# Kernel optimization log

Measured on AMD Instinct MI355X. Metric: run time of the kernel, lower is better.

Reference implementation:

```python
import jax, jax.numpy as jnp
import numpy as np
from itertools import permutations, combinations

BATCH = 32768
EPS = 1e-06  # positivity eps from __init__


def _levi_civita7():
    e = np.zeros((7,) * 7, dtype=np.float32)
    for p in permutations(range(7)):
        inv = sum(1 for i in range(7) for j in range(i + 1, 7) if p[i] > p[j])
        e[p] = -1.0 if inv % 2 else 1.0
    return jnp.asarray(e)

_EPS7 = _levi_civita7()  # (7,7,7,7,7,7,7) rank-7 Levi-Civita tensor
_TRIPLES = np.array(list(combinations(range(7), 3)), dtype=np.int32)  # (35,3) i<j<k index triples
_PERMS3 = [((0, 1, 2), 1.0), ((1, 2, 0), 1.0), ((2, 0, 1), 1.0),
           ((0, 2, 1), -1.0), ((2, 1, 0), -1.0), ((1, 0, 2), -1.0)]


def _phi_full(phi):
    # expand 35 independent components to fully antisymmetric (B,7,7,7)
    b = phi.shape[0]
    pf = jnp.zeros((b, 7, 7, 7), phi.dtype)
    for perm, s in _PERMS3:
        ia = _TRIPLES[:, perm[0]]
        ib = _TRIPLES[:, perm[1]]
        ic = _TRIPLES[:, perm[2]]
        pf = pf.at[:, ia, ib, ic].set(s * phi)
    return pf


def _metric_from_phi(phi):
    # Standard G2 metric: B_ij = (1/144) phi_ikl phi_jmn phi_pqr eps^{klmnpqr};
    # g = B / |det B|^{1/9}  (unit-determinant normalization)
    pf = _phi_full(phi)  # (B,7,7,7)
    C = jnp.einsum('klmnpqr,bpqr->bklmn', _EPS7, pf)  # (B,7,7,7,7)
    T = jnp.einsum('bklmn,bjmn->bklj', C, pf)          # (B,7,7,7)
    Bm = jnp.einsum('bikl,bklj->bij', pf, T) / 144.0   # (B,7,7)
    det = jnp.linalg.det(Bm)
    g = Bm / (jnp.abs(det)[:, None, None] + 1e-12) ** (1.0 / 9.0)
    return 0.5 * (g + jnp.swapaxes(g, -1, -2))  # exact symmetry for eigvalsh


def setup_inputs() -> dict:
    key = jax.random.key(0)
    phi = jax.random.normal(key, (BATCH, 35), dtype=jnp.float32)
    return {"phi": phi}


def reference(phi):
    g = _metric_from_phi(phi)              # (B,7,7)
    ev = jnp.linalg.eigvalsh(g)            # (B,7)
    return jax.nn.relu(-ev + EPS).sum(axis=-1)  # (B,) sum of negative-eigenvalue violations
```

## Files before the change

kernel.cpp:

```cpp
#include <hip/hip_runtime.h>
#include <utility>

#define BATCH 32768
#define NPHI 35
#define SWEEPS 6

constexpr int choose2(int n){ return (n*(n-1))/2; }

constexpr int tri_id_sorted(int a,int b,int c){
  int id=0;
  for(int x=0;x<a;++x) id += choose2(6-x);
  for(int y=a+1;y<b;++y) id += (6-y);
  id += (c-b-1);
  return id;
}

constexpr int tri_id3(int a,int b,int c){
  int x=a,y=b,z=c;
  if (x>y){int t=x;x=y;y=t;}
  if (y>z){int t=y;y=z;z=t;}
  if (x>y){int t=x;x=y;y=t;}
  return tri_id_sorted(x,y,z);
}

constexpr int sgn3(int a,int b,int c){
  int inv = (a>b)+(a>c)+(b>c);
  return (inv&1)? -1 : 1;
}

constexpr int UT(int i,int j){
  return i*7 - (i*(i-1))/2 + (j-i);
}

constexpr int pair_k(int g){
  int idx=0;
  for(int k=0;k<7;++k) for(int l=k+1;l<7;++l){ if(idx==g) return k; ++idx; }
  return 0;
}
constexpr int pair_l(int g){
  int idx=0;
  for(int k=0;k<7;++k) for(int l=k+1;l<7;++l){ if(idx==g) return l; ++idx; }
  return 0;
}

constexpr int rr_p(int r,int s){ int a=(r+1+s)%7, b=(r+6-s)%7; return a<b?a:b; }
constexpr int rr_q(int r,int s){ int a=(r+1+s)%7, b=(r+6-s)%7; return a<b?b:a; }

struct GProg {
  int nt, nb;
  signed char t_dst[50], t_a[50], t_b[50], t_s[50]; unsigned char t_init[50];
  signed char b_dst[26], b_a[26], b_b[26], b_s[26];
};

constexpr GProg build_group(int k,int l){
  GProg P{}; P.nt=0; P.nb=0;
  bool tinit[7]={};
  for(int m=0;m<7;++m) for(int n2=m+1;n2<7;++n2){
    if(m==k||m==l||n2==k||n2==l) continue;
    int comp[3]={0,0,0}; int cn=0;
    for(int x=0;x<7;++x) if(x!=k&&x!=l&&x!=m&&x!=n2){ comp[cn]=x; ++cn; }
    int perm[7]={k,l,m,n2,comp[0],comp[1],comp[2]};
    int invc=0;
    for(int i=0;i<7;++i) for(int j=i+1;j<7;++j) if(perm[i]>perm[j]) ++invc;
    const int es=(invc&1)? -1 : 1;
    const int tcomp=tri_id_sorted(comp[0],comp[1],comp[2]);
    for(int j=0;j<7;++j){
      if(j==m||j==n2) continue;
      P.t_dst[P.nt]=(signed char)j;
      P.t_a [P.nt]=(signed char)tcomp;
      P.t_b [P.nt]=(signed char)tri_id3(j,m,n2);
      P.t_s [P.nt]=(signed char)(es*sgn3(j,m,n2));
      P.t_init[P.nt]=tinit[j]?0:1; tinit[j]=true;
      ++P.nt;
    }
  }
  for(int i=0;i<7;++i){
    if(i==k||i==l) continue;
    for(int j=i;j<7;++j){
      P.b_dst[P.nb]=(signed char)UT(i,j);
      P.b_a [P.nb]=(signed char)tri_id3(i,k,l);
      P.b_b [P.nb]=(signed char)j;
      P.b_s [P.nb]=(signed char)sgn3(i,k,l);
      ++P.nb;
    }
  }
  return P;
}

template<int G> inline constexpr GProg GP = build_group(pair_k(G), pair_l(G));

template<int G,int Q>
__device__ __forceinline__ void t_step(float (&T)[7], const float (&ph)[NPHI]){
  constexpr int d=GP<G>.t_dst[Q], a=GP<G>.t_a[Q], b=GP<G>.t_b[Q];
  constexpr bool neg=(GP<G>.t_s[Q]<0), ini=(GP<G>.t_init[Q]!=0);
  const float x = neg ? -ph[a] : ph[a];
  if constexpr (ini) T[d] = x*ph[b];
  else               T[d] = fmaf(x, ph[b], T[d]);
}

template<int G,int Q>
__device__ __forceinline__ void b_step(float (&U)[28], const float (&T)[7],
                                       const float (&ph)[NPHI]){
  constexpr int d=GP<G>.b_dst[Q], a=GP<G>.b_a[Q], b=GP<G>.b_b[Q];
  constexpr bool neg=(GP<G>.b_s[Q]<0);
  const float x = neg ? -ph[a] : ph[a];
  U[d] = fmaf(x, T[b], U[d]);
}

template<int G,int... TQ>
__device__ __forceinline__ void run_t(float (&T)[7], const float (&ph)[NPHI],
                                      std::integer_sequence<int,TQ...>){
  (t_step<G,TQ>(T,ph), ...);
}
template<int G,int... BQ>
__device__ __forceinline__ void run_b(float (&U)[28], const float (&T)[7],
                                      const float (&ph)[NPHI],
                                      std::integer_sequence<int,BQ...>){
  (b_step<G,BQ>(U,T,ph), ...);
}

template<int G>
__device__ __forceinline__ void do_group(float (&U)[28], const float (&ph)[NPHI]){
  float T[7];
  run_t<G>(T, ph, std::make_integer_sequence<int, GP<G>.nt>{});
  run_b<G>(U, T, ph, std::make_integer_sequence<int, GP<G>.nb>{});
  __builtin_amdgcn_sched_barrier(0);
}

template<int... G>
__device__ __forceinline__ void all_groups(float (&U)[28], const float (&ph)[NPHI],
                                           std::integer_sequence<int,G...>){
  (do_group<G>(U,ph), ...);
}

template<int P,int Q>
__device__ __forceinline__ void jangle(const float (&A)[28],
                                       float &t, float &c, float &s){
  const float apq = A[UT(P,Q)];
  const float app = A[UT(P,P)];
  const float aqq = A[UT(Q,Q)];
  const float s2  = apq + apq;
  const float h   = aqq - app;
  const float r   = __builtin_amdgcn_sqrtf(fmaf(s2, s2, h*h));
  const float den = h + __builtin_copysignf(r + 1e-38f, h);
  t = s2 * __builtin_amdgcn_rcpf(den);
  c = __builtin_amdgcn_rsqf(fmaf(t, t, 1.0f));
  s = t*c;
}

template<int P,int Q>
__device__ __forceinline__ void japply(float (&A)[28], float t, float c, float s){
  const float apq = A[UT(P,Q)];
  A[UT(P,P)] = fmaf(-t, apq, A[UT(P,P)]);
  A[UT(Q,Q)] = fmaf( t, apq, A[UT(Q,Q)]);
  A[UT(P,Q)] = 0.0f;
  #pragma unroll
  for (int r2=0;r2<7;++r2){
    if (r2==P || r2==Q) continue;
    const int irp = (r2<P)? UT(r2,P) : UT(P,r2);
    const int irq = (r2<Q)? UT(r2,Q) : UT(Q,r2);
    const float arp = A[irp], arq = A[irq];
    A[irp] = fmaf(c, arp, -(s*arq));
    A[irq] = fmaf(c, arq,  (s*arp));
  }
}

template<int R>
__device__ __forceinline__ void jround(float (&A)[28]){
  constexpr int p0=rr_p(R,0), q0=rr_q(R,0);
  constexpr int p1=rr_p(R,1), q1=rr_q(R,1);
  constexpr int p2=rr_p(R,2), q2=rr_q(R,2);
  float t0,c0,s0, t1,c1,s1, t2,c2,s2;
  jangle<p0,q0>(A, t0,c0,s0);
  jangle<p1,q1>(A, t1,c1,s1);
  jangle<p2,q2>(A, t2,c2,s2);
  japply<p0,q0>(A, t0,c0,s0);
  japply<p1,q1>(A, t1,c1,s1);
  japply<p2,q2>(A, t2,c2,s2);
}

template<int... R>
__device__ __forceinline__ void jsweep(float (&A)[28],
                                       std::integer_sequence<int,R...>){
  (jround<R>(A), ...);
}

__device__ __forceinline__ float finish(const float (&A)[28]){
  float det = 1.0f;
  #pragma unroll
  for (int i=0;i<7;++i) det *= A[UT(i,i)];
  const float ad = fabsf(det) + 1e-12f;
  const float scale = __builtin_amdgcn_exp2f(__builtin_amdgcn_logf(ad) * (1.0f/9.0f));
  const float inv = __builtin_amdgcn_rcpf(scale);
  float sum = 0.0f;
  #pragma unroll
  for (int i=0;i<7;++i){
    const float ev = A[UT(i,i)]*inv;
    sum += fmaxf(1e-6f - ev, 0.0f);
  }
  return sum;
}

__global__ __launch_bounds__(64,1)
void PositivityConstraint_89086211654295_kernel(const float* __restrict__ phi,
                                                float* __restrict__ out){
  const int lane = threadIdx.x;
  const int gid  = blockIdx.x*64 + lane;

  __shared__ float lph[64*36];
  const float* __restrict__ gbase = phi + (size_t)blockIdx.x * 64 * NPHI;
  #pragma unroll
  for (int i=0;i<NPHI;++i){
    const int idx = i*64 + lane;
    lph[(idx/NPHI)*36 + (idx%NPHI)] = gbase[idx];
  }
  __syncthreads();

  float ph[NPHI];
  #pragma unroll
  for (int i=0;i<NPHI;++i) ph[i] = lph[lane*36 + i];

  float U[28];
  #pragma unroll
  for (int i=0;i<28;++i) U[i]=0.f;

  all_groups(U, ph, std::make_integer_sequence<int,21>{});

  float A[28];
  #pragma unroll
  for (int i=0;i<28;++i) A[i] = U[i]*(1.0f/6.0f);

  for (int sweep=0; sweep<SWEEPS; ++sweep){
    jsweep(A, std::make_integer_sequence<int,7>{});
  }

  out[gid] = finish(A);
}

extern "C" void kernel_launch(void* const* d_in, const int* in_sizes, int n_in,
                              void* d_out, int out_size, void* d_ws, size_t ws_size,
                              hipStream_t stream) {
  const float* phi = (const float*)d_in[0];
  float* out = (float*)d_out;
  (void)in_sizes; (void)n_in; (void)out_size; (void)d_ws; (void)ws_size;
  hipLaunchKernelGGL(PositivityConstraint_89086211654295_kernel,
                     dim3(BATCH/64), dim3(64), 0, stream, phi, out);
}
```

Baseline: 66.23 us.

## Split metric polynomial across four waves and move Jacobi into a separate kernel

The kernel is split in two. The first kernel spreads the 21 pair-groups of the cubic metric polynomial across four wavefronts per 64-element block, sums the partial 28-entry upper triangles in shared memory, and writes them to a workspace buffer. The second kernel loads each triangle with float4 reads and runs the Jacobi eigenvalue sweeps. This raises parallelism in the polynomial stage, since the original launched only 512 single-wave blocks. The cost is a second launch, a global round trip for the intermediate matrices, and a shared-memory reduction.

```diff
diff --git a/kernel.cpp b/kernel.cpp
--- a/kernel.cpp
+++ b/kernel.cpp
@@ -127,10 +127,59 @@
   __builtin_amdgcn_sched_barrier(0);
 }
 
-template<int... G>
-__device__ __forceinline__ void all_groups(float (&U)[28], const float (&ph)[NPHI],
-                                           std::integer_sequence<int,G...>){
-  (do_group<G>(U,ph), ...);
+template<int G0,int... I>
+__device__ __forceinline__ void groups_range_impl(float (&U)[28], const float (&ph)[NPHI],
+                                                  std::integer_sequence<int,I...>){
+  (do_group<G0+I>(U,ph), ...);
+}
+template<int G0,int G1>
+__device__ __forceinline__ void groups_range(float (&U)[28], const float (&ph)[NPHI]){
+  groups_range_impl<G0>(U, ph, std::make_integer_sequence<int, G1-G0>{});
+}
+
+__global__ __launch_bounds__(256,1)
+void PositivityConstraint_poly_kernel(const float* __restrict__ phi,
+                                      float* __restrict__ bws){
+  const int t    = threadIdx.x;
+  const int wv   = t >> 6;
+  const int lane = t & 63;
+  const int eblk = blockIdx.x * 64;
+
+  __shared__ float lph[64*36];
+  __shared__ float part[4*64*29];
+
+  const float* __restrict__ gbase = phi + (size_t)eblk * NPHI;
+  for (int i = t; i < 64*NPHI; i += 256){
+    lph[(i/NPHI)*36 + (i%NPHI)] = gbase[i];
+  }
+  __syncthreads();
+
+  float ph[NPHI];
+  #pragma unroll
+  for (int i=0;i<NPHI;++i) ph[i] = lph[lane*36 + i];
+
+  float U[28];
+  #pragma unroll
+  for (int i=0;i<28;++i) U[i]=0.f;
+
+  if      (wv==0) groups_range<0,5>(U, ph);
+  else if (wv==1) groups_range<5,10>(U, ph);
+  else if (wv==2) groups_range<10,15>(U, ph);
+  else            groups_range<15,21>(U, ph);
+
+  #pragma unroll
+  for (int i=0;i<28;++i) part[(wv*64 + lane)*29 + i] = U[i];
+  __syncthreads();
+
+  const int e = t >> 2, c = t & 3;
+  float* __restrict__ dst = bws + (size_t)blockIdx.x*1792 + e*28 + c*7;
+  #pragma unroll
+  for (int j=0;j<7;++j){
+    const int i = c*7 + j;
+    const float s = part[(0*64+e)*29 + i] + part[(1*64+e)*29 + i]
+                  + part[(2*64+e)*29 + i] + part[(3*64+e)*29 + i];
+    dst[j] = s;
+  }
 }
 
 template<int P,int Q>
@@ -202,33 +251,21 @@
 }
 
 __global__ __launch_bounds__(64,1)
-void PositivityConstraint_89086211654295_kernel(const float* __restrict__ phi,
+void PositivityConstraint_89086211654295_kernel(const float* __restrict__ bws,
                                                 float* __restrict__ out){
-  const int lane = threadIdx.x;
-  const int gid  = blockIdx.x*64 + lane;
-
-  __shared__ float lph[64*36];
-  const float* __restrict__ gbase = phi + (size_t)blockIdx.x * 64 * NPHI;
-  #pragma unroll
-  for (int i=0;i<NPHI;++i){
-    const int idx = i*64 + lane;
-    lph[(idx/NPHI)*36 + (idx%NPHI)] = gbase[idx];
-  }
-  __syncthreads();
-
-  float ph[NPHI];
-  #pragma unroll
-  for (int i=0;i<NPHI;++i) ph[i] = lph[lane*36 + i];
-
-  float U[28];
-  #pragma unroll
-  for (int i=0;i<28;++i) U[i]=0.f;
-
-  all_groups(U, ph, std::make_integer_sequence<int,21>{});
-
+  const int gid = blockIdx.x*64 + threadIdx.x;
+
+  const float4* __restrict__ src =
+      reinterpret_cast<const float4*>(bws + (size_t)gid * 28);
   float A[28];
   #pragma unroll
-  for (int i=0;i<28;++i) A[i] = U[i]*(1.0f/6.0f);
+  for (int k=0;k<7;++k){
+    const float4 v = src[k];
+    A[4*k+0] = v.x*(1.0f/6.0f);
+    A[4*k+1] = v.y*(1.0f/6.0f);
+    A[4*k+2] = v.z*(1.0f/6.0f);
+    A[4*k+3] = v.w*(1.0f/6.0f);
+  }
 
   for (int sweep=0; sweep<SWEEPS; ++sweep){
     jsweep(A, std::make_integer_sequence<int,7>{});
@@ -242,7 +279,11 @@
                               hipStream_t stream) {
   const float* phi = (const float*)d_in[0];
   float* out = (float*)d_out;
-  (void)in_sizes; (void)n_in; (void)out_size; (void)d_ws; (void)ws_size;
+  float* bws = (float*)d_ws;
+  (void)in_sizes; (void)n_in; (void)out_size; (void)ws_size;
+
+  hipLaunchKernelGGL(PositivityConstraint_poly_kernel,
+                     dim3(BATCH/64), dim3(256), 0, stream, phi, bws);
   hipLaunchKernelGGL(PositivityConstraint_89086211654295_kernel,
-                     dim3(BATCH/64), dim3(64), 0, stream, phi, out);
-}
+                     dim3(BATCH/64), dim3(64), 0, stream, bws, out);
+}
```

Measured after the change: 69.27 us. 1.05x slower.
